# Optimization experiments

Measured on AMD Instinct MI355X. Metric: run time of the kernel, lower is better.

Reference implementation:

```python
import jax, jax.numpy as jnp
import numpy as np

D_MODEL = 1024
N_HEADS = 16
HEAD_DIM = D_MODEL // N_HEADS
WINDOW = 128
NEG = -1e9


def setup_inputs() -> dict:
    key = jax.random.key(0)
    ks = jax.random.split(key, 9)
    s = 1.0 / np.sqrt(D_MODEL)
    x = jax.random.normal(ks[0], (1, 4096, D_MODEL), dtype=jnp.float32)
    Wq = jax.random.uniform(ks[1], (D_MODEL, D_MODEL), jnp.float32, -s, s)
    bq = jax.random.uniform(ks[2], (D_MODEL,), jnp.float32, -s, s)
    Wk = jax.random.uniform(ks[3], (D_MODEL, D_MODEL), jnp.float32, -s, s)
    bk = jax.random.uniform(ks[4], (D_MODEL,), jnp.float32, -s, s)
    Wv = jax.random.uniform(ks[5], (D_MODEL, D_MODEL), jnp.float32, -s, s)
    bv = jax.random.uniform(ks[6], (D_MODEL,), jnp.float32, -s, s)
    Wo = jax.random.uniform(ks[7], (D_MODEL, D_MODEL), jnp.float32, -s, s)
    bo = jax.random.uniform(ks[8], (D_MODEL,), jnp.float32, -s, s)
    return {"x": x, "Wq": Wq, "bq": bq, "Wk": Wk, "bk": bk,
            "Wv": Wv, "bv": bv, "Wo": Wo, "bo": bo}


def reference(x, Wq, bq, Wk, bk, Wv, bv, Wo, bo):
    B, S, _ = x.shape
    scale = 1.0 / np.sqrt(HEAD_DIM)

    def heads(W, b):
        # [B,S,D] -> [B,H,S,hd]  (torch Linear: x @ W.T + b)
        return (x @ W.T + b).reshape(B, S, N_HEADS, HEAD_DIM).transpose(0, 2, 1, 3)

    q = heads(Wq, bq)
    k = heads(Wk, bk)
    v = heads(Wv, bv)

    scores = jnp.einsum('bhqd,bhkd->bhqk', q, k) * scale  # [B,H,S,S]
    i = jnp.arange(S)
    window_mask = jnp.abs(i[:, None] - i[None, :]) <= (WINDOW // 2)  # [S,S]
    scores = jnp.where(window_mask[None, None], scores, NEG)
    attn = jax.nn.softmax(scores, axis=-1)
    ctx = jnp.einsum('bhqk,bhkd->bhqd', attn, v)
    ctx = ctx.transpose(0, 2, 1, 3).reshape(B, S, D_MODEL)
    return ctx @ Wo.T + bo
```

## Files before the change

### kernel.cpp

```cpp
#include <hip/hip_runtime.h>
#include <type_traits>

typedef __bf16 bf16;
typedef __bf16 bf16x8 __attribute__((ext_vector_type(8)));
typedef __bf16 bf16x4 __attribute__((ext_vector_type(4)));
typedef float floatx4 __attribute__((ext_vector_type(4)));

#define SEQ 4096
#define DM 1024
#define NH 16
#define HD 64
#define GUARD 64

__device__ __forceinline__ floatx4 mfma32(bf16x8 a, bf16x8 b, floatx4 c) {
    return __builtin_amdgcn_mfma_f32_16x16x32_bf16(a, b, c, 0, 0, 0);
}

__device__ __forceinline__ bf16x8 load8(const bf16* p) {
    return *(const bf16x8*)p;
}

__device__ __forceinline__ void async_ld16(const bf16* g, bf16* l) {
    __builtin_amdgcn_global_load_lds(
        (const __attribute__((address_space(1))) unsigned int*)g,
        (__attribute__((address_space(3))) unsigned int*)l,
        16, 0, 0);
}

__global__ __launch_bounds__(256) void prep_kernel(
    const float* __restrict__ x,  const float* __restrict__ Wq,
    const float* __restrict__ Wk, const float* __restrict__ Wv,
    const float* __restrict__ Wo, const float* __restrict__ bq,
    const float* __restrict__ bk, const float* __restrict__ bv,
    bf16* __restrict__ xb, bf16* __restrict__ Wcat,
    bf16* __restrict__ Wob, float* __restrict__ bcat)
{
    const int WN8 = 131072;
    const int XN8 = 524288;
    int b = blockIdx.x;
    if (b == 4096) {
        for (int k = threadIdx.x; k < 3 * DM; k += 256)
            bcat[k] = k < DM ? bq[k] : (k < 2 * DM ? bk[k - DM] : bv[k - 2 * DM]);
        return;
    }
    int c = b * 256 + threadIdx.x;
    const float* src; bf16* dst;
    if (c < XN8)              { src = x;  dst = xb; }
    else if (c < XN8 + WN8)   { src = Wq; dst = Wcat;                 c -= XN8; }
    else if (c < XN8 + 2*WN8) { src = Wk; dst = Wcat + (size_t)DM*DM;     c -= XN8 + WN8; }
    else if (c < XN8 + 3*WN8) { src = Wv; dst = Wcat + (size_t)2*DM*DM;   c -= XN8 + 2*WN8; }
    else                      { src = Wo; dst = Wob;                  c -= XN8 + 3*WN8; }
    float4 a = ((const float4*)src)[2 * c], d2 = ((const float4*)src)[2 * c + 1];
    bf16x8 o;
    o[0] = (bf16)a.x;  o[1] = (bf16)a.y;  o[2] = (bf16)a.z;  o[3] = (bf16)a.w;
    o[4] = (bf16)d2.x; o[5] = (bf16)d2.y; o[6] = (bf16)d2.z; o[7] = (bf16)d2.w;
    *(bf16x8*)(dst + 8 * (size_t)c) = o;
}

__global__ __launch_bounds__(256, 3) void gemm_qkv_kernel(
    const bf16* __restrict__ A,
    const bf16* __restrict__ B,
    const float* __restrict__ bias,
    bf16* __restrict__ Qh, bf16* __restrict__ Kh, bf16* __restrict__ Vt)
{
    constexpr int K = DM;
    __shared__ bf16 As[128 * 64];
    __shared__ bf16 Bs[128 * 64];

    const int tid  = threadIdx.x;
    const int wave = tid >> 6;
    const int lane = tid & 63;
    const int l15  = lane & 15;
    const int quad = lane >> 4;
    const int m0 = blockIdx.x * 128;
    const int n0 = blockIdx.y * 128;
    const int wm = (wave & 1) * 64;
    const int wn = (wave >> 1) * 64;

    const int lr = lane >> 3;
    const int gc = ((lane & 7) - lr) & 7;

    const bf16* aptr[4]; bf16* alds[4];
    const bf16* bptr[4]; bf16* blds[4];
#pragma unroll
    for (int i = 0; i < 4; ++i) {
        int ci = wave + 4 * i;
        aptr[i] = A + (size_t)(m0 + ci * 8 + lr) * K + gc * 8;
        alds[i] = As + ci * 512;
        bptr[i] = B + (size_t)(n0 + ci * 8 + lr) * K + gc * 8;
        blds[i] = Bs + ci * 512;
    }

    floatx4 acc[4][4] = {};
    const int sw0 = (quad + (l15 & 7)) & 7;
    const bool qk = (n0 < 2 * DM);

    auto kloop = [&](auto swtag) {
        constexpr bool SW = decltype(swtag)::value;
        for (int k0 = 0; k0 < K; k0 += 64) {
            __syncthreads();
#pragma unroll
            for (int i = 0; i < 4; ++i) async_ld16(aptr[i] + k0, alds[i]);
#pragma unroll
            for (int i = 0; i < 4; ++i) async_ld16(bptr[i] + k0, blds[i]);
            __syncthreads();
#pragma unroll
            for (int h = 0; h < 2; ++h) {
                const int so = ((sw0 + 4 * h) & 7) * 8;
                bf16x8 af[4], bfr[4];
#pragma unroll
                for (int i = 0; i < 4; ++i)
                    af[i] = load8(As + (wm + i * 16 + l15) * 64 + so);
#pragma unroll
                for (int j = 0; j < 4; ++j)
                    bfr[j] = load8(Bs + (wn + j * 16 + l15) * 64 + so);
#pragma unroll
                for (int i = 0; i < 4; ++i)
#pragma unroll
                    for (int j = 0; j < 4; ++j)
                        acc[i][j] = SW ? mfma32(bfr[j], af[i], acc[i][j])
                                       : mfma32(af[i], bfr[j], acc[i][j]);
            }
        }
    };
    if (qk) kloop(std::true_type{}); else kloop(std::false_type{});

    const int nb = n0 + wn;
    if (qk) {
        bf16* dst = (nb < DM) ? Qh : Kh;
        const int hh = ((nb < DM) ? nb : nb - DM) >> 6;
#pragma unroll
        for (int i = 0; i < 4; ++i) {
            int s = m0 + wm + i * 16 + l15;
            bf16* row = dst + ((size_t)hh * SEQ + s) * 64;
#pragma unroll
            for (int j = 0; j < 4; ++j) {
                int d4 = j * 16 + quad * 4;
                float4 bv = *(const float4*)(bias + nb + d4);
                bf16x4 o = {(bf16)(acc[i][j][0] + bv.x), (bf16)(acc[i][j][1] + bv.y),
                            (bf16)(acc[i][j][2] + bv.z), (bf16)(acc[i][j][3] + bv.w)};
                *(bf16x4*)(row + d4) = o;
            }
        }
    } else {
#pragma unroll
        for (int j = 0; j < 4; ++j) {
            int vrow = (nb - 2 * DM) + j * 16 + l15;
            float bvs = bias[nb + j * 16 + l15];
            bf16* row = Vt + (size_t)vrow * SEQ;
#pragma unroll
            for (int i = 0; i < 4; ++i) {
                int s4 = m0 + wm + i * 16 + quad * 4;
                bf16x4 o = {(bf16)(acc[i][j][0] + bvs), (bf16)(acc[i][j][1] + bvs),
                            (bf16)(acc[i][j][2] + bvs), (bf16)(acc[i][j][3] + bvs)};
                *(bf16x4*)(row + s4) = o;
            }
        }
    }
}

template <int BM, typename TOUT>
__global__ __launch_bounds__(256, 4) void gemm_sw_kernel(
    const bf16* __restrict__ A, const bf16* __restrict__ B,
    const float* __restrict__ bias, TOUT* __restrict__ C,
    int M, int N, int K)
{
    constexpr int MI = BM / 32;
    __shared__ bf16 As[BM * 64];
    __shared__ bf16 Bs[128 * 64];

    const int tid  = threadIdx.x;
    const int wave = tid >> 6;
    const int lane = tid & 63;
    const int l15  = lane & 15;
    const int quad = lane >> 4;
    const int m0 = blockIdx.x * BM;
    const int n0 = blockIdx.y * 128;
    const int wm = (wave & 1) * (BM / 2);
    const int wn = (wave >> 1) * 64;

    const int lr = lane >> 3;
    const int gc = ((lane & 7) - lr) & 7;

    const bf16* aptr[MI]; bf16* alds[MI];
    const bf16* bptr[4];  bf16* blds[4];
#pragma unroll
    for (int i = 0; i < MI; ++i) {
        int ci = wave + 4 * i;
        aptr[i] = A + (size_t)(m0 + ci * 8 + lr) * K + gc * 8;
        alds[i] = As + ci * 512;
    }
#pragma unroll
    for (int j = 0; j < 4; ++j) {
        int cj = wave + 4 * j;
        bptr[j] = B + (size_t)(n0 + cj * 8 + lr) * K + gc * 8;
        blds[j] = Bs + cj * 512;
    }

    floatx4 acc[MI][4] = {};
    const int sw0 = (quad + (l15 & 7)) & 7;

    for (int k0 = 0; k0 < K; k0 += 64) {
        __syncthreads();
#pragma unroll
        for (int i = 0; i < MI; ++i) async_ld16(aptr[i] + k0, alds[i]);
#pragma unroll
        for (int j = 0; j < 4; ++j) async_ld16(bptr[j] + k0, blds[j]);
        __syncthreads();
#pragma unroll
        for (int h = 0; h < 2; ++h) {
            const int so = ((sw0 + 4 * h) & 7) * 8;
            bf16x8 af[MI], bfr[4];
#pragma unroll
            for (int i = 0; i < MI; ++i)
                af[i] = load8(As + (wm + i * 16 + l15) * 64 + so);
#pragma unroll
            for (int j = 0; j < 4; ++j)
                bfr[j] = load8(Bs + (wn + j * 16 + l15) * 64 + so);
#pragma unroll
            for (int i = 0; i < MI; ++i)
#pragma unroll
                for (int j = 0; j < 4; ++j)
                    acc[i][j] = mfma32(bfr[j], af[i], acc[i][j]);
        }
    }

#pragma unroll
    for (int i = 0; i < MI; ++i) {
        int xm = m0 + wm + i * 16 + l15;
#pragma unroll
        for (int j = 0; j < 4; ++j) {
            int cn = n0 + wn + j * 16 + quad * 4;
            float4 bv = *(const float4*)(bias + cn);
            float v0 = acc[i][j][0] + bv.x;
            float v1 = acc[i][j][1] + bv.y;
            float v2 = acc[i][j][2] + bv.z;
            float v3 = acc[i][j][3] + bv.w;
            if constexpr (sizeof(TOUT) == 2) {
                bf16x4 o = {(bf16)v0, (bf16)v1, (bf16)v2, (bf16)v3};
                *(bf16x4*)((bf16*)C + (size_t)xm * N + cn) = o;
            } else {
                float4 o = {v0, v1, v2, v3};
                *(float4*)((float*)C + (size_t)xm * N + cn) = o;
            }
        }
    }
}

__global__ __launch_bounds__(256) void swattn_kernel(
    const bf16* __restrict__ Qh, const bf16* __restrict__ Kh,
    const bf16* __restrict__ Vt, bf16* __restrict__ ctx)
{
    __shared__ bf16 Pc[4][16][40];
    __shared__ float lred[4][16];

    const int tid  = threadIdx.x;
    const int wave = tid >> 6;
    const int lane = tid & 63;
    const int l15  = lane & 15;
    const int quad = lane >> 4;
    const int q0   = blockIdx.x * 64;
    const int h    = blockIdx.y;
    const int hoff = h * HD;

    const bf16* qhead = Qh + (size_t)h * SEQ * 64;
    const bf16* khead = Kh + (size_t)h * SEQ * 64;
    const bf16* vhead = Vt + (size_t)hoff * SEQ;

    const int qrow = q0 + wave * 16 + l15;
    bf16x8 aq0 = load8(qhead + (size_t)qrow * 64 + quad * 8);
    bf16x8 aq1 = load8(qhead + (size_t)qrow * 64 + quad * 8 + 32);

    const int ws = q0 - 64 + wave * 16;
    floatx4 s[9];
#pragma unroll
    for (int st = 0; st < 9; ++st) {
        int kr = ws + st * 16 + l15;
        int kc2 = kr < 0 ? 0 : (kr > SEQ - 1 ? SEQ - 1 : kr);
        const bf16* kp = khead + (size_t)kc2 * 64 + quad * 8;
        bf16x8 b0 = load8(kp), b1 = load8(kp + 32);
        floatx4 acc = {};
        acc = mfma32(aq0, b0, acc);
        acc = mfma32(aq1, b1, acc);
        s[st] = acc;
    }

#pragma unroll
    for (int r = 0; r < 4; ++r) {
        int row = quad * 4 + r;
        float mx = -INFINITY;
#pragma unroll
        for (int st = 0; st < 9; ++st) {
            int j = st * 16 + l15;
            int gk = ws + j;
            bool ok = (j >= row) && (j <= 128 + row) && (gk >= 0) && (gk < SEQ);
            float v = ok ? s[st][r] * 0.125f : -1e30f;
            s[st][r] = v;
            mx = fmaxf(mx, v);
        }
        mx = fmaxf(mx, __shfl_xor(mx, 1));
        mx = fmaxf(mx, __shfl_xor(mx, 2));
        mx = fmaxf(mx, __shfl_xor(mx, 4));
        mx = fmaxf(mx, __shfl_xor(mx, 8));
        float sum = 0.f;
#pragma unroll
        for (int st = 0; st < 9; ++st) {
            float p = __expf(s[st][r] - mx);
            s[st][r] = p;
            sum += p;
        }
        sum += __shfl_xor(sum, 1);
        sum += __shfl_xor(sum, 2);
        sum += __shfl_xor(sum, 4);
        sum += __shfl_xor(sum, 8);
        lred[wave][row] = sum;
    }

    floatx4 ot[4] = {};
#pragma unroll
    for (int kc = 0; kc < 5; ++kc) {
#pragma unroll
        for (int r = 0; r < 4; ++r) {
            int row = quad * 4 + r;
            Pc[wave][row][l15] = (bf16)s[2 * kc][r];
            Pc[wave][row][16 + l15] = (kc < 4) ? (bf16)s[2 * kc + 1][r] : (bf16)0.f;
        }
        bf16x8 pb = load8(&Pc[wave][l15][quad * 8]);
#pragma unroll
        for (int dt = 0; dt < 4; ++dt) {
            const bf16* vp = vhead + (ptrdiff_t)(dt * 16 + l15) * SEQ
                                   + (ptrdiff_t)(ws + kc * 32 + quad * 8);
            ot[dt] = mfma32(load8(vp), pb, ot[dt]);
        }
    }

    float linv = 1.0f / lred[wave][l15];
#pragma unroll
    for (int dt = 0; dt < 4; ++dt) {
        bf16x4 o4;
#pragma unroll
        for (int r = 0; r < 4; ++r) o4[r] = (bf16)(ot[dt][r] * linv);
        *(bf16x4*)(ctx + (size_t)qrow * DM + hoff + dt * 16 + quad * 4) = o4;
    }
}

extern "C" void kernel_launch(void* const* d_in, const int* in_sizes, int n_in,
                              void* d_out, int out_size, void* d_ws, size_t ws_size,
                              hipStream_t stream) {
    const float* x  = (const float*)d_in[0];
    const float* Wq = (const float*)d_in[1];
    const float* bq = (const float*)d_in[2];
    const float* Wk = (const float*)d_in[3];
    const float* bk = (const float*)d_in[4];
    const float* Wv = (const float*)d_in[5];
    const float* bv = (const float*)d_in[6];
    const float* Wo = (const float*)d_in[7];
    const float* bo = (const float*)d_in[8];
    float* out = (float*)d_out;

    const size_t XN = (size_t)SEQ * DM;
    const size_t WN = (size_t)DM * DM;

    bf16* xb    = (bf16*)d_ws;
    bf16* Wcat  = xb + XN;
    bf16* Wob   = Wcat + 3 * WN;
    bf16* Qh    = Wob + WN;
    bf16* Kh    = Qh + XN;
    bf16* VtRaw = Kh + XN;
    bf16* Vtb   = VtRaw + GUARD;
    float* bcat = (float*)(VtRaw + XN + 2 * GUARD + 128);
    bf16* ctx   = xb;

    prep_kernel<<<4097, 256, 0, stream>>>(x, Wq, Wk, Wv, Wo, bq, bk, bv,
                                          xb, Wcat, Wob, bcat);

    gemm_qkv_kernel<<<dim3(SEQ / 128, 24), 256, 0, stream>>>(
        xb, Wcat, bcat, Qh, Kh, Vtb);

    swattn_kernel<<<dim3(SEQ / 64, NH), 256, 0, stream>>>(Qh, Kh, Vtb, ctx);

    gemm_sw_kernel<64, float><<<dim3(SEQ / 64, DM / 128), 256, 0, stream>>>(
        ctx, Wob, bo, out, SEQ, DM, DM);
}
```

Baseline: 161.0 us.

## Stage K window in LDS for attention and enlarge output GEMM tile

The attention kernel now loads the block's 224-row K window cooperatively into padded shared memory once, so the four waves read overlapping K rows from LDS instead of each fetching them separately from global memory. The output projection GEMM drops its template for a fixed 128x128 tile with compile-time sizes and launch bounds of 3. That halves the grid to 256 blocks, which raises reuse per block but may leave some compute units idle.

```diff
diff --git a/kernel.cpp b/kernel.cpp
--- a/kernel.cpp
+++ b/kernel.cpp
@@ -159,14 +159,12 @@
     }
 }
 
-template <int BM, typename TOUT>
-__global__ __launch_bounds__(256, 4) void gemm_sw_kernel(
+__global__ __launch_bounds__(256, 3) void gemm_out_kernel(
     const bf16* __restrict__ A, const bf16* __restrict__ B,
-    const float* __restrict__ bias, TOUT* __restrict__ C,
-    int M, int N, int K)
+    const float* __restrict__ bias, float* __restrict__ C)
 {
-    constexpr int MI = BM / 32;
-    __shared__ bf16 As[BM * 64];
+    constexpr int K = DM, N = DM;
+    __shared__ bf16 As[128 * 64];
     __shared__ bf16 Bs[128 * 64];
 
     const int tid  = threadIdx.x;
@@ -174,51 +172,47 @@
     const int lane = tid & 63;
     const int l15  = lane & 15;
     const int quad = lane >> 4;
-    const int m0 = blockIdx.x * BM;
+    const int m0 = blockIdx.x * 128;
     const int n0 = blockIdx.y * 128;
-    const int wm = (wave & 1) * (BM / 2);
+    const int wm = (wave & 1) * 64;
     const int wn = (wave >> 1) * 64;
 
     const int lr = lane >> 3;
     const int gc = ((lane & 7) - lr) & 7;
 
-    const bf16* aptr[MI]; bf16* alds[MI];
-    const bf16* bptr[4];  bf16* blds[4];
-#pragma unroll
-    for (int i = 0; i < MI; ++i) {
+    const bf16* aptr[4]; bf16* alds[4];
+    const bf16* bptr[4]; bf16* blds[4];
+#pragma unroll
+    for (int i = 0; i < 4; ++i) {
         int ci = wave + 4 * i;
         aptr[i] = A + (size_t)(m0 + ci * 8 + lr) * K + gc * 8;
         alds[i] = As + ci * 512;
-    }
-#pragma unroll
-    for (int j = 0; j < 4; ++j) {
-        int cj = wave + 4 * j;
-        bptr[j] = B + (size_t)(n0 + cj * 8 + lr) * K + gc * 8;
-        blds[j] = Bs + cj * 512;
-    }
-
-    floatx4 acc[MI][4] = {};
+        bptr[i] = B + (size_t)(n0 + ci * 8 + lr) * K + gc * 8;
+        blds[i] = Bs + ci * 512;
+    }
+
+    floatx4 acc[4][4] = {};
     const int sw0 = (quad + (l15 & 7)) & 7;
 
     for (int k0 = 0; k0 < K; k0 += 64) {
         __syncthreads();
 #pragma unroll
-        for (int i = 0; i < MI; ++i) async_ld16(aptr[i] + k0, alds[i]);
-#pragma unroll
-        for (int j = 0; j < 4; ++j) async_ld16(bptr[j] + k0, blds[j]);
+        for (int i = 0; i < 4; ++i) async_ld16(aptr[i] + k0, alds[i]);
+#pragma unroll
+        for (int i = 0; i < 4; ++i) async_ld16(bptr[i] + k0, blds[i]);
         __syncthreads();
 #pragma unroll
         for (int h = 0; h < 2; ++h) {
             const int so = ((sw0 + 4 * h) & 7) * 8;
-            bf16x8 af[MI], bfr[4];
-#pragma unroll
-            for (int i = 0; i < MI; ++i)
+            bf16x8 af[4], bfr[4];
+#pragma unroll
+            for (int i = 0; i < 4; ++i)
                 af[i] = load8(As + (wm + i * 16 + l15) * 64 + so);
 #pragma unroll
             for (int j = 0; j < 4; ++j)
                 bfr[j] = load8(Bs + (wn + j * 16 + l15) * 64 + so);
 #pragma unroll
-            for (int i = 0; i < MI; ++i)
+            for (int i = 0; i < 4; ++i)
 #pragma unroll
                 for (int j = 0; j < 4; ++j)
                     acc[i][j] = mfma32(bfr[j], af[i], acc[i][j]);
@@ -226,31 +220,24 @@
     }
 
 #pragma unroll
-    for (int i = 0; i < MI; ++i) {
+    for (int i = 0; i < 4; ++i) {
         int xm = m0 + wm + i * 16 + l15;
 #pragma unroll
         for (int j = 0; j < 4; ++j) {
             int cn = n0 + wn + j * 16 + quad * 4;
             float4 bv = *(const float4*)(bias + cn);
-            float v0 = acc[i][j][0] + bv.x;
-            float v1 = acc[i][j][1] + bv.y;
-            float v2 = acc[i][j][2] + bv.z;
-            float v3 = acc[i][j][3] + bv.w;
-            if constexpr (sizeof(TOUT) == 2) {
-                bf16x4 o = {(bf16)v0, (bf16)v1, (bf16)v2, (bf16)v3};
-                *(bf16x4*)((bf16*)C + (size_t)xm * N + cn) = o;
-            } else {
-                float4 o = {v0, v1, v2, v3};
-                *(float4*)((float*)C + (size_t)xm * N + cn) = o;
-            }
-        }
-    }
-}
-
-__global__ __launch_bounds__(256) void swattn_kernel(
+            float4 o = {acc[i][j][0] + bv.x, acc[i][j][1] + bv.y,
+                        acc[i][j][2] + bv.z, acc[i][j][3] + bv.w};
+            *(float4*)(C + (size_t)xm * N + cn) = o;
+        }
+    }
+}
+
+__global__ __launch_bounds__(256, 4) void swattn_kernel(
     const bf16* __restrict__ Qh, const bf16* __restrict__ Kh,
     const bf16* __restrict__ Vt, bf16* __restrict__ ctx)
 {
+    __shared__ bf16 Ks[224 * 72];
     __shared__ bf16 Pc[4][16][40];
     __shared__ float lred[4][16];
 
@@ -262,23 +249,35 @@
     const int q0   = blockIdx.x * 64;
     const int h    = blockIdx.y;
     const int hoff = h * HD;
+    const int kbase = q0 - 64;
 
     const bf16* qhead = Qh + (size_t)h * SEQ * 64;
     const bf16* khead = Kh + (size_t)h * SEQ * 64;
     const bf16* vhead = Vt + (size_t)hoff * SEQ;
 
+#pragma unroll
+    for (int it = 0; it < 7; ++it) {
+        int task = tid + it * 256;
+        int row = task >> 3, chunk = task & 7;
+        int gk = kbase + row;
+        gk = gk < 0 ? 0 : (gk > SEQ - 1 ? SEQ - 1 : gk);
+        bf16x8 v = load8(khead + (size_t)gk * 64 + chunk * 8);
+        *(bf16x8*)&Ks[row * 72 + chunk * 8] = v;
+    }
+
     const int qrow = q0 + wave * 16 + l15;
     bf16x8 aq0 = load8(qhead + (size_t)qrow * 64 + quad * 8);
     bf16x8 aq1 = load8(qhead + (size_t)qrow * 64 + quad * 8 + 32);
 
-    const int ws = q0 - 64 + wave * 16;
+    __syncthreads();
+
+    const int ws = kbase + wave * 16;
     floatx4 s[9];
 #pragma unroll
     for (int st = 0; st < 9; ++st) {
-        int kr = ws + st * 16 + l15;
-        int kc2 = kr < 0 ? 0 : (kr > SEQ - 1 ? SEQ - 1 : kr);
-        const bf16* kp = khead + (size_t)kc2 * 64 + quad * 8;
-        bf16x8 b0 = load8(kp), b1 = load8(kp + 32);
+        const bf16* kp = &Ks[((wave + st) * 16 + l15) * 72 + quad * 8];
+        bf16x8 b0 = load8(kp);
+        bf16x8 b1 = load8(kp + 32);
         floatx4 acc = {};
         acc = mfma32(aq0, b0, acc);
         acc = mfma32(aq1, b1, acc);
@@ -379,6 +378,6 @@
 
     swattn_kernel<<<dim3(SEQ / 64, NH), 256, 0, stream>>>(Qh, Kh, Vtb, ctx);
 
-    gemm_sw_kernel<64, float><<<dim3(SEQ / 64, DM / 128), 256, 0, stream>>>(
-        ctx, Wob, bo, out, SEQ, DM, DM);
-}
+    gemm_out_kernel<<<dim3(SEQ / 128, DM / 128), 256, 0, stream>>>(
+        ctx, Wob, bo, out);
+}
```

Measured after the change: 166.0 us. +3.1%, slower.
